# Kernel optimization log

Measured on AMD Instinct MI355X. Metric: run time of the kernel, lower is better.

## Reference

```python
import jax, jax.numpy as jnp
import numpy as np

B, N, L, H, V, LAYERS = 512, 32, 50, 256, 100000, 1


def setup_inputs() -> dict:
    key = jax.random.key(0)
    ks = jax.random.split(key, 18)
    std = 1.0 / np.sqrt(H)
    u = lambda k, shape: jax.random.uniform(k, shape, jnp.float32, -std, std)
    return {
        # forward args
        "A": jax.random.uniform(ks[0], (B, N, 2 * N), jnp.float32),
        "items": jax.random.randint(ks[1], (B, N), 0, V + 1),
        "seq_alias": jax.random.randint(ks[2], (B, L), 0, N),
        "mask": jnp.ones((B, L), jnp.int32),
        # learned parameters (uniform(-1/sqrt(H), 1/sqrt(H)) as in the module)
        "emb": u(ks[3], (V + 1, H)),
        "W_in": u(ks[4], (H, H)), "b_in": u(ks[5], (H,)),
        "W_out": u(ks[6], (H, H)), "b_out": u(ks[7], (H,)),
        "W_ih": u(ks[8], (2 * H, 3 * H)), "b_ih": u(ks[9], (3 * H,)),
        "W_hh": u(ks[10], (H, 3 * H)), "b_hh": u(ks[11], (3 * H,)),
        "fc1_w": u(ks[12], (H, H)), "fc1_b": u(ks[13], (H,)),
        "fc2_w": u(ks[14], (H, H)), "fc2_b": u(ks[15], (H,)),
        "fc3_w": u(ks[16], (H, 1)),
    }


def reference(A, items, seq_alias, mask, emb, W_in, b_in, W_out, b_out,
              W_ih, b_ih, W_hh, b_hh, fc1_w, fc1_b, fc2_w, fc2_b, fc3_w):
    # --- GGNN over dense batched adjacency A: [B, N, 2N] ---
    h = emb[items]  # [B, N, H]
    for _ in range(LAYERS):
        m_in = jnp.einsum('bij,bjh->bih', A[:, :, :N], h @ W_in + b_in)
        m_out = jnp.einsum('bij,bjh->bih', A[:, :, N:], h @ W_out + b_out)
        a = jnp.concatenate([m_in, m_out], axis=-1)  # [B, N, 2H]
        # torch.nn.GRUCell math
        gi = a @ W_ih + b_ih  # [B, N, 3H]
        gh = h @ W_hh + b_hh
        i_r, i_z, i_n = jnp.split(gi, 3, axis=-1)
        h_r, h_z, h_n = jnp.split(gh, 3, axis=-1)
        r = jax.nn.sigmoid(i_r + h_r)
        z = jax.nn.sigmoid(i_z + h_z)
        ng = jnp.tanh(i_n + r * h_n)
        h = ng + z * (h - ng)
    # --- per-sample gather of session sequences (vectorized embed_seq) ---
    h_seqs = jnp.take_along_axis(h, seq_alias[:, :, None], axis=1)  # [B, L, H]
    tail = mask.sum(axis=1) - 1  # index of last valid position
    h_tail = jnp.take_along_axis(h_seqs, tail[:, None, None], axis=1)[:, 0]  # [B, H]
    # --- attention pooling ---
    q1 = (h_tail @ fc1_w + fc1_b)[:, None, :]  # [B, 1, H]
    q2 = h_seqs @ fc2_w + fc2_b                # [B, L, H]
    alpha = jax.nn.sigmoid(q1 + q2) @ fc3_w    # [B, L, 1]
    seq_emb = jnp.sum(alpha * h_seqs * mask[:, :, None].astype(h.dtype), axis=1)  # [B, H]
    # --- score against all items (excluding padding row 0) ---
    return seq_emb @ emb[1:].T  # [B, V]
```

## Files before the change

### kernel.cpp

```cpp
#include <hip/hip_runtime.h>
#include <cmath>

#define HH 256
#define NB 32
#define LSEQ 50
#define BB 512
#define VOC 100000
#define VPAD 100032

typedef __attribute__((ext_vector_type(8))) short short8;
typedef __attribute__((ext_vector_type(4))) float f32x4;

static __device__ __forceinline__ unsigned short f2bf(float x) {
  unsigned u = __builtin_bit_cast(unsigned, x);
  u = (u + 0x7fff + ((u >> 16) & 1)) >> 16;
  return (unsigned short)u;
}
static __device__ __forceinline__ float bf2f(unsigned short h) {
  unsigned u = ((unsigned)h) << 16;
  return __builtin_bit_cast(float, u);
}
static __device__ __forceinline__ uint2 pack_hi4(float4 x, uint2& pl) {
  const unsigned short h0 = f2bf(x.x), h1 = f2bf(x.y), h2 = f2bf(x.z), h3 = f2bf(x.w);
  const unsigned short l0 = f2bf(x.x - bf2f(h0)), l1 = f2bf(x.y - bf2f(h1));
  const unsigned short l2 = f2bf(x.z - bf2f(h2)), l3 = f2bf(x.w - bf2f(h3));
  uint2 ph;
  ph.x = (unsigned)h0 | ((unsigned)h1 << 16);
  ph.y = (unsigned)h2 | ((unsigned)h3 << 16);
  pl.x = (unsigned)l0 | ((unsigned)l1 << 16);
  pl.y = (unsigned)l2 | ((unsigned)l3 << 16);
  return ph;
}

static __device__ __forceinline__ void cp16(void* lds, const void* g) {
  __builtin_amdgcn_global_load_lds(
      (const __attribute__((address_space(1))) unsigned int*)g,
      (__attribute__((address_space(3))) unsigned int*)lds, 16, 0, 0);
}

__global__ void prep_weights(const float* __restrict__ W_in, const float* __restrict__ b_in,
                             const float* __restrict__ W_out, const float* __restrict__ b_out,
                             const float* __restrict__ W_hh, const float* __restrict__ b_hh,
                             const float* __restrict__ W_ih, const float* __restrict__ fc2_w,
                             unsigned short* __restrict__ Wt_all, float* __restrict__ b_all,
                             unsigned short* __restrict__ WihT, unsigned short* __restrict__ fc2T)
{
  const int bid = blockIdx.x, k = threadIdx.x;
  if (bid < 1280) {
    const float* src; const float* bsrc; int col, nc;
    if (bid < 256)      { src = W_in;  bsrc = b_in;  col = bid;       nc = 256; }
    else if (bid < 512) { src = W_out; bsrc = b_out; col = bid - 256; nc = 256; }
    else                { src = W_hh;  bsrc = b_hh;  col = bid - 512; nc = 768; }
    Wt_all[bid * 256 + k] = f2bf(src[k * nc + col]);
    if (k == 0) b_all[bid] = bsrc[col];
  } else if (bid < 2048) {
    const int n = bid - 1280;
    WihT[n * 512 + k]       = f2bf(W_ih[k * 768 + n]);
    WihT[n * 512 + k + 256] = f2bf(W_ih[(k + 256) * 768 + n]);
  } else {
    const int n = bid - 2048;
    fc2T[n * 256 + k] = f2bf(fc2_w[k * 256 + n]);
  }
}

__global__ __launch_bounds__(256) void embsplit(const float* __restrict__ emb,
                                                unsigned short* __restrict__ ehi,
                                                unsigned short* __restrict__ elo)
{
  const int idx4 = blockIdx.x * 256 + threadIdx.x;
  const int v = idx4 >> 6, c4 = idx4 & 63;
  float4 x = make_float4(0.f, 0.f, 0.f, 0.f);
  if (v < VOC) x = *(const float4*)&emb[(size_t)(v + 1) * HH + c4 * 4];
  uint2 pl;
  const uint2 ph = pack_hi4(x, pl);
  *(uint2*)&ehi[(size_t)v * HH + c4 * 4] = ph;
  *(uint2*)&elo[(size_t)v * HH + c4 * 4] = pl;
}

__global__ __launch_bounds__(256, 3) void gemm_asplit_nt(
    const unsigned short* __restrict__ Ah, const unsigned short* __restrict__ Al,
    const unsigned short* __restrict__ Bt, const float* __restrict__ bias,
    float* __restrict__ C, int N, int K, int ldc)
{
  __shared__ unsigned short sAh[4 * 128 * 8];
  __shared__ unsigned short sAl[4 * 128 * 8];
  __shared__ unsigned short sB [4 * 128 * 8];
  const int tid = threadIdx.x;
  const int n0 = blockIdx.x * 128, m0 = blockIdx.y * 128;
  const int lane = tid & 63, wave = tid >> 6;
  const int quad = lane >> 4, l16 = lane & 15;
  const int wm = (wave >> 1) * 64, wn = (wave & 1) * 64;

  f32x4 acc[4][4];
#pragma unroll
  for (int i = 0; i < 4; ++i)
#pragma unroll
    for (int j = 0; j < 4; ++j)
#pragma unroll
      for (int r = 0; r < 4; ++r) acc[i][j][r] = 0.f;

  const int c0 = tid, c1 = tid + 256;
  const int q0 = c0 >> 7, r0 = c0 & 127;
  const int q1c = c1 >> 7, r1 = c1 & 127;

  for (int k0 = 0; k0 < K; k0 += 32) {
    const size_t ga0 = (size_t)(m0 + r0) * K + k0 + q0 * 8;
    const size_t ga1 = (size_t)(m0 + r1) * K + k0 + q1c * 8;
    const size_t gb0 = (size_t)(n0 + r0) * K + k0 + q0 * 8;
    const size_t gb1 = (size_t)(n0 + r1) * K + k0 + q1c * 8;
    cp16(&sAh[c0 * 8], &Ah[ga0]);
    cp16(&sAh[c1 * 8], &Ah[ga1]);
    cp16(&sAl[c0 * 8], &Al[ga0]);
    cp16(&sAl[c1 * 8], &Al[ga1]);
    cp16(&sB [c0 * 8], &Bt[gb0]);
    cp16(&sB [c1 * 8], &Bt[gb1]);
    __syncthreads();

    short8 fah[4], fal[4];
#pragma unroll
    for (int ms = 0; ms < 4; ++ms) {
      const int row = wm + ms * 16 + l16;
      fah[ms] = *(const short8*)&sAh[(quad * 128 + row) * 8];
      fal[ms] = *(const short8*)&sAl[(quad * 128 + row) * 8];
    }
#pragma unroll
    for (int ns = 0; ns < 4; ++ns) {
      const int col = wn + ns * 16 + l16;
      const short8 fb = *(const short8*)&sB[(quad * 128 + col) * 8];
#pragma unroll
      for (int ms = 0; ms < 4; ++ms) {
        acc[ms][ns] = __builtin_amdgcn_mfma_f32_16x16x32_bf16(fah[ms], fb, acc[ms][ns], 0, 0, 0);
        acc[ms][ns] = __builtin_amdgcn_mfma_f32_16x16x32_bf16(fal[ms], fb, acc[ms][ns], 0, 0, 0);
      }
    }
    __syncthreads();
  }

#pragma unroll
  for (int ns = 0; ns < 4; ++ns) {
    const int n = n0 + wn + ns * 16 + l16;
    const float bv = bias[n];
#pragma unroll
    for (int ms = 0; ms < 4; ++ms) {
      const int mrow = m0 + wm + ms * 16 + quad * 4;
#pragma unroll
      for (int r = 0; r < 4; ++r)
        C[(size_t)(mrow + r) * ldc + n] = acc[ms][ns][r] + bv;
    }
  }
}

#define TS 64
#define KSTEP 16
#define LDPF 68
__global__ __launch_bounds__(256) void gemm_nn_bias(
    const float* __restrict__ A, const float* __restrict__ W,
    const float* __restrict__ bias, float* __restrict__ C,
    int M, int N, int K)
{
  __shared__ float As[KSTEP * LDPF];
  __shared__ float Ws[KSTEP * LDPF];
  const int tid = threadIdx.x;
  const int tx = tid & 15, ty = tid >> 4;
  const int n0 = blockIdx.x * TS, m0 = blockIdx.y * TS;
  const int lkk = tid & 15, lm = tid >> 4;
  const int ln  = tid & 63, lkr = tid >> 6;
  float acc[4][4] = {};
  for (int k0 = 0; k0 < K; k0 += KSTEP) {
#pragma unroll
    for (int r = 0; r < 4; ++r)
      As[lkk * LDPF + lm + r * 16] = A[(m0 + lm + r * 16) * K + k0 + lkk];
#pragma unroll
    for (int r = 0; r < 4; ++r)
      Ws[(lkr + r * 4) * LDPF + ln] = W[(k0 + lkr + r * 4) * N + n0 + ln];
    __syncthreads();
#pragma unroll
    for (int kk = 0; kk < KSTEP; ++kk) {
      const float4 a4 = *(const float4*)(As + kk * LDPF + ty * 4);
      const float4 w4 = *(const float4*)(Ws + kk * LDPF + tx * 4);
      const float av[4] = {a4.x, a4.y, a4.z, a4.w};
      const float wv[4] = {w4.x, w4.y, w4.z, w4.w};
#pragma unroll
      for (int i = 0; i < 4; ++i)
#pragma unroll
        for (int j = 0; j < 4; ++j)
          acc[i][j] += av[i] * wv[j];
    }
    __syncthreads();
  }
  const float4 b4 = *(const float4*)(bias + n0 + tx * 4);
  const float bv[4] = {b4.x, b4.y, b4.z, b4.w};
#pragma unroll
  for (int i = 0; i < 4; ++i) {
    float4 o;
    o.x = acc[i][0] + bv[0]; o.y = acc[i][1] + bv[1];
    o.z = acc[i][2] + bv[2]; o.w = acc[i][3] + bv[3];
    *(float4*)(C + (m0 + ty * 4 + i) * N + n0 + tx * 4) = o;
  }
}

__global__ void gather_h0(const int* __restrict__ items, const float* __restrict__ emb,
                          float* __restrict__ h0, unsigned short* __restrict__ h0h,
                          unsigned short* __restrict__ h0l, int total4)
{
  const int e = blockIdx.x * blockDim.x + threadIdx.x;
  if (e >= total4) return;
  const int row = e >> 6, c = e & 63;
  const int it = items[row];
  const float4 x = ((const float4*)emb)[it * 64 + c];
  ((float4*)h0)[e] = x;
  uint2 pl;
  const uint2 ph = pack_hi4(x, pl);
  *(uint2*)&h0h[e * 4] = ph;
  *(uint2*)&h0l[e * 4] = pl;
}

__global__ __launch_bounds__(256) void msg_kernel(
    const float* __restrict__ A, const float* __restrict__ C1,
    unsigned short* __restrict__ ach, unsigned short* __restrict__ acl)
{
  const int b = blockIdx.x;
  const int tid = threadIdx.x;
  __shared__ float Ash[NB * 64];
#pragma unroll
  for (int r = 0; r < 8; ++r)
    Ash[tid + r * 256] = A[b * (NB * 2 * NB) + tid + r * 256];
  float hi[NB], ho[NB];
#pragma unroll
  for (int j = 0; j < NB; ++j) {
    hi[j] = C1[(size_t)(b * NB + j) * 1280 + tid];
    ho[j] = C1[(size_t)(b * NB + j) * 1280 + 256 + tid];
  }
  __syncthreads();
  for (int i = 0; i < NB; ++i) {
    float si = 0.f, so = 0.f;
#pragma unroll
    for (int j = 0; j < NB; ++j) {
      si += Ash[i * 64 + j] * hi[j];
      so += Ash[i * 64 + 32 + j] * ho[j];
    }
    const int idx = (b * NB + i) * 512 + tid;
    const unsigned short sh = f2bf(si);
    ach[idx] = sh; acl[idx] = f2bf(si - bf2f(sh));
    const unsigned short oh = f2bf(so);
    ach[idx + 256] = oh; acl[idx + 256] = f2bf(so - bf2f(oh));
  }
}

__global__ void gru_kernel(const float* __restrict__ gi, const float* __restrict__ C1,
                           float* __restrict__ h, int total)
{
  const int idx = blockIdx.x * blockDim.x + threadIdx.x;
  if (idx >= total) return;
  const int row = idx >> 8, k = idx & 255;
  const float* gir = gi + (size_t)row * 768;
  const float* ghr = C1 + (size_t)row * 1280 + 512;
  const float ir = gir[k], iz = gir[k + 256], inn = gir[k + 512];
  const float hr = ghr[k], hz = ghr[k + 256], hn = ghr[k + 512];
  const float r = 1.f / (1.f + expf(-(ir + hr)));
  const float z = 1.f / (1.f + expf(-(iz + hz)));
  const float n = tanhf(inn + r * hn);
  const float h0v = h[idx];
  h[idx] = n + z * (h0v - n);
}

__global__ __launch_bounds__(256) void seq_gather2(
    const int* __restrict__ seq_alias, const int* __restrict__ mask,
    const float* __restrict__ h, float* __restrict__ h_seqs,
    unsigned short* __restrict__ hsh, unsigned short* __restrict__ hsl,
    float* __restrict__ h_tail)
{
  const int b = blockIdx.x, tid = threadIdx.x;
  __shared__ int tail_sh;
  if (tid < 64) {
    int s = (tid < LSEQ) ? mask[b * LSEQ + tid] : 0;
#pragma unroll
    for (int off = 32; off > 0; off >>= 1) s += __shfl_down(s, off, 64);
    if (tid == 0) tail_sh = s - 1;
  }
  __syncthreads();
  const int tail = tail_sh;
  const int l0 = blockIdx.y * 10;
  for (int l = l0; l < l0 + 10; ++l) {
    const int al = seq_alias[b * LSEQ + l];
    const float v = h[(size_t)(b * NB + al) * HH + tid];
    const int idx = (b * LSEQ + l) * HH + tid;
    h_seqs[idx] = v;
    const unsigned short vh = f2bf(v);
    hsh[idx] = vh; hsl[idx] = f2bf(v - bf2f(vh));
    if (l == tail) h_tail[b * HH + tid] = v;
  }
}

__global__ __launch_bounds__(256) void attn_kernel2(
    const float* __restrict__ q1, const float* __restrict__ q2,
    const float* __restrict__ fc3_w, const float* __restrict__ h_seqs,
    const int* __restrict__ mask, float* __restrict__ seq_emb)
{
  const int b = blockIdx.x;
  const int tid = threadIdx.x, wave = tid >> 6, lane = tid & 63;
  __shared__ float red[4 * HH];
  const float4 q1v = *(const float4*)&q1[b * HH + lane * 4];
  const float4 w3v = *(const float4*)&fc3_w[lane * 4];
  float4 acc = make_float4(0.f, 0.f, 0.f, 0.f);
  for (int l = wave; l < LSEQ; l += 4) {
    if (!mask[b * LSEQ + l]) continue;
    const float4 q2v = *(const float4*)&q2[(size_t)(b * LSEQ + l) * HH + lane * 4];
    float s = (1.f / (1.f + expf(-(q1v.x + q2v.x)))) * w3v.x
            + (1.f / (1.f + expf(-(q1v.y + q2v.y)))) * w3v.y
            + (1.f / (1.f + expf(-(q1v.z + q2v.z)))) * w3v.z
            + (1.f / (1.f + expf(-(q1v.w + q2v.w)))) * w3v.w;
#pragma unroll
    for (int off = 32; off > 0; off >>= 1) s += __shfl_xor(s, off, 64);
    const float4 hv = *(const float4*)&h_seqs[(size_t)(b * LSEQ + l) * HH + lane * 4];
    acc.x += s * hv.x; acc.y += s * hv.y; acc.z += s * hv.z; acc.w += s * hv.w;
  }
  *(float4*)&red[wave * HH + lane * 4] = acc;
  __syncthreads();
  const float r = red[tid] + red[HH + tid] + red[2 * HH + tid] + red[3 * HH + tid];
  seq_emb[b * HH + tid] = r;
}

__global__ void split_seq(const float* __restrict__ s, unsigned short* __restrict__ hi,
                          unsigned short* __restrict__ lo, int n)
{
  const int i = blockIdx.x * blockDim.x + threadIdx.x;
  if (i >= n) return;
  const float x = s[i];
  const unsigned short h = f2bf(x);
  hi[i] = h;
  lo[i] = f2bf(x - bf2f(h));
}

__global__ __launch_bounds__(256, 4) void scorer_presplit(
    const unsigned short* __restrict__ seq_hi,
    const unsigned short* __restrict__ seq_lo,
    const unsigned short* __restrict__ ehi,
    const unsigned short* __restrict__ elo,
    float* __restrict__ out)
{
  const int tid = threadIdx.x;
  const int m0 = blockIdx.x * 256;
  const int v0 = blockIdx.y * 64;
  const int lane = tid & 63, wave = tid >> 6;
  const int quad = lane >> 4, l16 = lane & 15;
  const int mwave = m0 + wave * 64;

  f32x4 acc[4][4];
#pragma unroll
  for (int i = 0; i < 4; ++i)
#pragma unroll
    for (int j = 0; j < 4; ++j)
#pragma unroll
      for (int r = 0; r < 4; ++r) acc[i][j][r] = 0.f;

#pragma unroll
  for (int ks = 0; ks < 8; ++ks) {
    const int kk = ks * 32 + quad * 8;
    short8 bh[4], bl[4];
#pragma unroll
    for (int vs = 0; vs < 4; ++vs) {
      const int boff = (v0 + vs * 16 + l16) * HH + kk;
      bh[vs] = *(const short8*)&ehi[boff];
      bl[vs] = *(const short8*)&elo[boff];
    }
#pragma unroll
    for (int ms = 0; ms < 4; ++ms) {
      const int aoff = (mwave + ms * 16 + l16) * HH + kk;
      const short8 ah = *(const short8*)&seq_hi[aoff];
      const short8 al = *(const short8*)&seq_lo[aoff];
#pragma unroll
      for (int vs = 0; vs < 4; ++vs) {
        acc[ms][vs] = __builtin_amdgcn_mfma_f32_16x16x32_bf16(ah, bh[vs], acc[ms][vs], 0, 0, 0);
        acc[ms][vs] = __builtin_amdgcn_mfma_f32_16x16x32_bf16(ah, bl[vs], acc[ms][vs], 0, 0, 0);
        acc[ms][vs] = __builtin_amdgcn_mfma_f32_16x16x32_bf16(al, bh[vs], acc[ms][vs], 0, 0, 0);
      }
    }
  }

#pragma unroll
  for (int ms = 0; ms < 4; ++ms) {
    const int mrow = mwave + ms * 16 + quad * 4;
#pragma unroll
    for (int vs = 0; vs < 4; ++vs) {
      const int v = v0 + vs * 16 + l16;
      if (v < VOC) {
#pragma unroll
        for (int r = 0; r < 4; ++r)
          out[(size_t)(mrow + r) * VOC + v] = acc[ms][vs][r];
      }
    }
  }
}

#define ELD2 136
__global__ __launch_bounds__(256, 3) void scorer_mfma(
    const unsigned short* __restrict__ seq_hi,
    const unsigned short* __restrict__ seq_lo,
    const float* __restrict__ emb,
    float* __restrict__ out)
{
  __shared__ unsigned short ehi[64 * ELD2];
  __shared__ unsigned short elo[64 * ELD2];
  const int tid = threadIdx.x;
  const int v0 = blockIdx.x * 64;
  const int m0 = blockIdx.y * 256;
  const int lane = tid & 63, wave = tid >> 6;
  const int quad = lane >> 4, l16 = lane & 15;
  const int mwave = m0 + wave * 64;

  f32x4 acc[4][4];
#pragma unroll
  for (int i = 0; i < 4; ++i)
#pragma unroll
    for (int j = 0; j < 4; ++j)
#pragma unroll
      for (int r = 0; r < 4; ++r) acc[i][j][r] = 0.f;

  for (int p = 0; p < 2; ++p) {
#pragma unroll
    for (int i = 0; i < 8; ++i) {
      const int idx4 = tid + i * 256;
      const int row = idx4 >> 5, c4 = idx4 & 31;
      const int v = v0 + row;
      float4 x = make_float4(0.f, 0.f, 0.f, 0.f);
      if (v < VOC) x = *(const float4*)&emb[(size_t)(v + 1) * HH + p * 128 + c4 * 4];
      uint2 pl;
      const uint2 ph = pack_hi4(x, pl);
      *(uint2*)&ehi[row * ELD2 + c4 * 4] = ph;
      *(uint2*)&elo[row * ELD2 + c4 * 4] = pl;
    }
    __syncthreads();

#pragma unroll
    for (int ks = 0; ks < 4; ++ks) {
      const int kk = ks * 32;
      short8 bh[4], bl[4];
#pragma unroll
      for (int vs = 0; vs < 4; ++vs) {
        const int off = (vs * 16 + l16) * ELD2 + kk + quad * 8;
        bh[vs] = *(const short8*)&ehi[off];
        bl[vs] = *(const short8*)&elo[off];
      }
#pragma unroll
      for (int ms = 0; ms < 4; ++ms) {
        const int m = mwave + ms * 16 + l16;
        const int aoff = m * HH + p * 128 + kk + quad * 8;
        const short8 ah = *(const short8*)&seq_hi[aoff];
        const short8 al = *(const short8*)&seq_lo[aoff];
#pragma unroll
        for (int vs = 0; vs < 4; ++vs) {
          acc[ms][vs] = __builtin_amdgcn_mfma_f32_16x16x32_bf16(ah, bh[vs], acc[ms][vs], 0, 0, 0);
          acc[ms][vs] = __builtin_amdgcn_mfma_f32_16x16x32_bf16(ah, bl[vs], acc[ms][vs], 0, 0, 0);
          acc[ms][vs] = __builtin_amdgcn_mfma_f32_16x16x32_bf16(al, bh[vs], acc[ms][vs], 0, 0, 0);
        }
      }
    }
    __syncthreads();
  }

#pragma unroll
  for (int ms = 0; ms < 4; ++ms) {
    const int mrow = mwave + ms * 16 + quad * 4;
#pragma unroll
    for (int vs = 0; vs < 4; ++vs) {
      const int v = v0 + vs * 16 + l16;
      if (v < VOC) {
#pragma unroll
        for (int r = 0; r < 4; ++r)
          out[(size_t)(mrow + r) * VOC + v] = acc[ms][vs][r];
      }
    }
  }
}

extern "C" void kernel_launch(void* const* d_in, const int* in_sizes, int n_in,
                              void* d_out, int out_size, void* d_ws, size_t ws_size,
                              hipStream_t stream)
{
  const float* A      = (const float*)d_in[0];
  const int* items    = (const int*)d_in[1];
  const int* seq_al   = (const int*)d_in[2];
  const int* mask     = (const int*)d_in[3];
  const float* emb    = (const float*)d_in[4];
  const float* W_in   = (const float*)d_in[5];
  const float* b_in   = (const float*)d_in[6];
  const float* W_out  = (const float*)d_in[7];
  const float* b_out  = (const float*)d_in[8];
  const float* W_ih   = (const float*)d_in[9];
  const float* b_ih   = (const float*)d_in[10];
  const float* W_hh   = (const float*)d_in[11];
  const float* b_hh   = (const float*)d_in[12];
  const float* fc1_w  = (const float*)d_in[13];
  const float* fc1_b  = (const float*)d_in[14];
  const float* fc2_w  = (const float*)d_in[15];
  const float* fc2_b  = (const float*)d_in[16];
  const float* fc3_w  = (const float*)d_in[17];
  float* out = (float*)d_out;

  float* ws = (float*)d_ws;
  float* h0      = ws;
  float* q1      = ws + 4194304;
  float* h_tail  = ws + 4325376;
  float* seq_emb = ws + 4456448;
  unsigned short* seq_hi = (unsigned short*)(ws + 4587520);
  unsigned short* seq_lo = (unsigned short*)(ws + 4653056);
  unsigned short* Wt_all = (unsigned short*)(ws + 4718592);
  unsigned short* WihT   = (unsigned short*)(ws + 4882432);
  unsigned short* fc2T   = (unsigned short*)(ws + 5079040);
  float* b_all   = ws + 5111808;
  unsigned short* emb_hi = (unsigned short*)(ws + 5113088);
  unsigned short* emb_lo = (unsigned short*)(ws + 5113088 + (size_t)VPAD * HH / 2);
  const bool presplit = ws_size >= ((size_t)5113088 * 4 + (size_t)VPAD * HH * 4);

  float* C1 = out;
  unsigned short* acat_h = (unsigned short*)(out + 20971520);
  unsigned short* acat_l = (unsigned short*)(out + 25165824);
  float* gi = out + 29360128;
  unsigned short* h0h = (unsigned short*)(out + 41943040);
  unsigned short* h0l = (unsigned short*)(out + 44040192);
  float* h_seqs = out;
  unsigned short* hs_h = (unsigned short*)(out + 6553600);
  unsigned short* hs_l = (unsigned short*)(out + 9830400);
  float* q2 = out + 13107200;

  const int MR = BB * NB;

  prep_weights<<<dim3(2304), dim3(256), 0, stream>>>(
      W_in, b_in, W_out, b_out, W_hh, b_hh, W_ih, fc2_w, Wt_all, b_all, WihT, fc2T);

  if (presplit)
    embsplit<<<dim3(VPAD * 64 / 256), dim3(256), 0, stream>>>(emb, emb_hi, emb_lo);

  gather_h0<<<dim3(MR * 64 / 256), dim3(256), 0, stream>>>(items, emb, h0, h0h, h0l, MR * 64);

  gemm_asplit_nt<<<dim3(1280 / 128, MR / 128), dim3(256), 0, stream>>>(
      h0h, h0l, Wt_all, b_all, C1, 1280, 256, 1280);

  msg_kernel<<<dim3(BB), dim3(256), 0, stream>>>(A, C1, acat_h, acat_l);

  gemm_asplit_nt<<<dim3(768 / 128, MR / 128), dim3(256), 0, stream>>>(
      acat_h, acat_l, WihT, b_ih, gi, 768, 512, 768);

  gru_kernel<<<dim3(MR * HH / 256), dim3(256), 0, stream>>>(gi, C1, h0, MR * HH);

  seq_gather2<<<dim3(BB, 5), dim3(256), 0, stream>>>(seq_al, mask, h0, h_seqs, hs_h, hs_l, h_tail);

  gemm_asplit_nt<<<dim3(256 / 128, (BB * LSEQ) / 128), dim3(256), 0, stream>>>(
      hs_h, hs_l, fc2T, fc2_b, q2, 256, 256, 256);

  gemm_nn_bias<<<dim3(HH / TS, BB / TS), dim3(256), 0, stream>>>(h_tail, fc1_w, fc1_b, q1, BB, HH, HH);

  attn_kernel2<<<dim3(BB), dim3(256), 0, stream>>>(q1, q2, fc3_w, h_seqs, mask, seq_emb);

  split_seq<<<dim3(BB * HH / 256), dim3(256), 0, stream>>>(seq_emb, seq_hi, seq_lo, BB * HH);

  if (presplit)
    scorer_presplit<<<dim3(2, (VOC + 63) / 64), dim3(256), 0, stream>>>(
        seq_hi, seq_lo, emb_hi, emb_lo, out);
  else
    scorer_mfma<<<dim3((VOC + 63) / 64, 2), dim3(256), 0, stream>>>(seq_hi, seq_lo, emb, out);
}
```

Baseline: 778.6 us.

## Stage pre-split embedding tiles in swizzled LDS for the scorer GEMM

The embedding split kernel now writes hi/lo bf16 halves in a tile-contiguous, XOR-swizzled layout of 64 rows per tile. The scorer copies each tile into shared memory in two K-halves with async 16-byte copies, so the second half loads while the first is being computed. B fragments then come from bank-conflict-free LDS reads instead of scattered global loads shared across all four waves. Grid order changes so adjacent blocks walk vocabulary tiles. The larger LDS footprint lowers occupancy to 2 blocks per SM.

After: 685.0 us. -12.0%, faster.

```diff
diff --git a/kernel.cpp b/kernel.cpp
--- a/kernel.cpp
+++ b/kernel.cpp
@@ -7,6 +7,7 @@
 #define BB 512
 #define VOC 100000
 #define VPAD 100032
+#define NTILE (VPAD / 64)
 
 typedef __attribute__((ext_vector_type(8))) short short8;
 typedef __attribute__((ext_vector_type(4))) float f32x4;
@@ -63,18 +64,31 @@
   }
 }
 
-__global__ __launch_bounds__(256) void embsplit(const float* __restrict__ emb,
-                                                unsigned short* __restrict__ ehi,
-                                                unsigned short* __restrict__ elo)
-{
-  const int idx4 = blockIdx.x * 256 + threadIdx.x;
-  const int v = idx4 >> 6, c4 = idx4 & 63;
-  float4 x = make_float4(0.f, 0.f, 0.f, 0.f);
-  if (v < VOC) x = *(const float4*)&emb[(size_t)(v + 1) * HH + c4 * 4];
-  uint2 pl;
-  const uint2 ph = pack_hi4(x, pl);
-  *(uint2*)&ehi[(size_t)v * HH + c4 * 4] = ph;
-  *(uint2*)&elo[(size_t)v * HH + c4 * 4] = pl;
+__global__ __launch_bounds__(256) void embsplit_t(const float* __restrict__ emb,
+                                                  unsigned short* __restrict__ ehiT,
+                                                  unsigned short* __restrict__ eloT)
+{
+  const int g = blockIdx.x * 256 + threadIdx.x;
+  const int u = g & 1023;
+  const int tp = g >> 10;
+  const int p = tp & 1, t = tp >> 1;
+  const int row = u >> 4, w = u & 15;
+  const int wp = w ^ (row & 7);
+  const int v = t * 64 + row;
+  float4 x0 = make_float4(0.f, 0.f, 0.f, 0.f), x1 = x0;
+  if (v < VOC) {
+    const float* s = &emb[(size_t)(v + 1) * HH + p * 128 + wp * 8];
+    x0 = *(const float4*)s;
+    x1 = *(const float4*)(s + 4);
+  }
+  uint2 l0, l1;
+  const uint2 h0 = pack_hi4(x0, l0);
+  const uint2 h1 = pack_hi4(x1, l1);
+  uint4 H, L;
+  H.x = h0.x; H.y = h0.y; H.z = h1.x; H.w = h1.y;
+  L.x = l0.x; L.y = l0.y; L.z = l1.x; L.w = l1.y;
+  *(uint4*)&ehiT[(size_t)g * 8] = H;
+  *(uint4*)&eloT[(size_t)g * 8] = L;
 }
 
 __global__ __launch_bounds__(256, 3) void gemm_asplit_nt(
@@ -332,16 +346,18 @@
   lo[i] = f2bf(x - bf2f(h));
 }
 
-__global__ __launch_bounds__(256, 4) void scorer_presplit(
+__global__ __launch_bounds__(256, 2) void scorer_split_lds(
     const unsigned short* __restrict__ seq_hi,
     const unsigned short* __restrict__ seq_lo,
-    const unsigned short* __restrict__ ehi,
-    const unsigned short* __restrict__ elo,
+    const unsigned short* __restrict__ ehiT,
+    const unsigned short* __restrict__ eloT,
     float* __restrict__ out)
 {
+  __shared__ unsigned short sH[2][8192];
+  __shared__ unsigned short sL[2][8192];
   const int tid = threadIdx.x;
-  const int m0 = blockIdx.x * 256;
-  const int v0 = blockIdx.y * 64;
+  const int t = blockIdx.x;
+  const int m0 = blockIdx.y * 256;
   const int lane = tid & 63, wave = tid >> 6;
   const int quad = lane >> 4, l16 = lane & 15;
   const int mwave = m0 + wave * 64;
@@ -354,30 +370,56 @@
 #pragma unroll
       for (int r = 0; r < 4; ++r) acc[i][j][r] = 0.f;
 
-#pragma unroll
-  for (int ks = 0; ks < 8; ++ks) {
-    const int kk = ks * 32 + quad * 8;
-    short8 bh[4], bl[4];
-#pragma unroll
-    for (int vs = 0; vs < 4; ++vs) {
-      const int boff = (v0 + vs * 16 + l16) * HH + kk;
-      bh[vs] = *(const short8*)&ehi[boff];
-      bl[vs] = *(const short8*)&elo[boff];
-    }
-#pragma unroll
-    for (int ms = 0; ms < 4; ++ms) {
-      const int aoff = (mwave + ms * 16 + l16) * HH + kk;
-      const short8 ah = *(const short8*)&seq_hi[aoff];
-      const short8 al = *(const short8*)&seq_lo[aoff];
-#pragma unroll
-      for (int vs = 0; vs < 4; ++vs) {
-        acc[ms][vs] = __builtin_amdgcn_mfma_f32_16x16x32_bf16(ah, bh[vs], acc[ms][vs], 0, 0, 0);
-        acc[ms][vs] = __builtin_amdgcn_mfma_f32_16x16x32_bf16(ah, bl[vs], acc[ms][vs], 0, 0, 0);
-        acc[ms][vs] = __builtin_amdgcn_mfma_f32_16x16x32_bf16(al, bh[vs], acc[ms][vs], 0, 0, 0);
-      }
-    }
-  }
-
+  const size_t tb = (size_t)t * 16384;
+
+#pragma unroll
+  for (int j = 0; j < 4; ++j) {
+    const int o = (tid + j * 256) * 8;
+    cp16(&sH[0][o], &ehiT[tb + o]);
+    cp16(&sL[0][o], &eloT[tb + o]);
+  }
+  __syncthreads();
+
+#pragma unroll
+  for (int j = 0; j < 4; ++j) {
+    const int o = (tid + j * 256) * 8;
+    cp16(&sH[1][o], &ehiT[tb + 8192 + o]);
+    cp16(&sL[1][o], &eloT[tb + 8192 + o]);
+  }
+
+#define SCORE_PHASE(D, P)                                                          \
+  {                                                                                \
+    _Pragma("unroll")                                                              \
+    for (int ks = 0; ks < 4; ++ks) {                                               \
+      const int kk = ks * 32;                                                      \
+      short8 bh[4], bl[4];                                                         \
+      _Pragma("unroll")                                                            \
+      for (int vs = 0; vs < 4; ++vs) {                                             \
+        const int row = vs * 16 + l16;                                             \
+        const int bo = (row * 256 + (kk + quad * 8) * 2) ^ ((row & 7) << 4);       \
+        bh[vs] = *(const short8*)((const char*)&sH[D][0] + bo);                    \
+        bl[vs] = *(const short8*)((const char*)&sL[D][0] + bo);                    \
+      }                                                                            \
+      _Pragma("unroll")                                                            \
+      for (int ms = 0; ms < 4; ++ms) {                                             \
+        const int aoff = (mwave + ms * 16 + l16) * HH + (P) * 128 + kk + quad * 8; \
+        const short8 ah = *(const short8*)&seq_hi[aoff];                           \
+        const short8 al = *(const short8*)&seq_lo[aoff];                           \
+        _Pragma("unroll")                                                          \
+        for (int vs = 0; vs < 4; ++vs) {                                           \
+          acc[ms][vs] = __builtin_amdgcn_mfma_f32_16x16x32_bf16(ah, bh[vs], acc[ms][vs], 0, 0, 0); \
+          acc[ms][vs] = __builtin_amdgcn_mfma_f32_16x16x32_bf16(ah, bl[vs], acc[ms][vs], 0, 0, 0); \
+          acc[ms][vs] = __builtin_amdgcn_mfma_f32_16x16x32_bf16(al, bh[vs], acc[ms][vs], 0, 0, 0); \
+        }                                                                          \
+      }                                                                            \
+    }                                                                              \
+  }
+
+  SCORE_PHASE(0, 0)
+  __syncthreads();
+  SCORE_PHASE(1, 1)
+
+  const int v0 = t * 64;
 #pragma unroll
   for (int ms = 0; ms < 4; ++ms) {
     const int mrow = mwave + ms * 16 + quad * 4;
@@ -391,6 +433,7 @@
       }
     }
   }
+#undef SCORE_PHASE
 }
 
 #define ELD2 136
@@ -489,8 +532,8 @@
   const float* b_out  = (const float*)d_in[8];
   const float* W_ih   = (const float*)d_in[9];
   const float* b_ih   = (const float*)d_in[10];
+  const float* b_hh   = (const float*)d_in[12];
   const float* W_hh   = (const float*)d_in[11];
-  const float* b_hh   = (const float*)d_in[12];
   const float* fc1_w  = (const float*)d_in[13];
   const float* fc1_b  = (const float*)d_in[14];
   const float* fc2_w  = (const float*)d_in[15];
@@ -509,8 +552,8 @@
   unsigned short* WihT   = (unsigned short*)(ws + 4882432);
   unsigned short* fc2T   = (unsigned short*)(ws + 5079040);
   float* b_all   = ws + 5111808;
-  unsigned short* emb_hi = (unsigned short*)(ws + 5113088);
-  unsigned short* emb_lo = (unsigned short*)(ws + 5113088 + (size_t)VPAD * HH / 2);
+  unsigned short* emb_hiT = (unsigned short*)(ws + 5113088);
+  unsigned short* emb_loT = (unsigned short*)(ws + 5113088 + (size_t)VPAD * HH / 2);
   const bool presplit = ws_size >= ((size_t)5113088 * 4 + (size_t)VPAD * HH * 4);
 
   float* C1 = out;
@@ -530,7 +573,7 @@
       W_in, b_in, W_out, b_out, W_hh, b_hh, W_ih, fc2_w, Wt_all, b_all, WihT, fc2T);
 
   if (presplit)
-    embsplit<<<dim3(VPAD * 64 / 256), dim3(256), 0, stream>>>(emb, emb_hi, emb_lo);
+    embsplit_t<<<dim3(NTILE * 8), dim3(256), 0, stream>>>(emb, emb_hiT, emb_loT);
 
   gather_h0<<<dim3(MR * 64 / 256), dim3(256), 0, stream>>>(items, emb, h0, h0h, h0l, MR * 64);
 
@@ -556,8 +599,8 @@
   split_seq<<<dim3(BB * HH / 256), dim3(256), 0, stream>>>(seq_emb, seq_hi, seq_lo, BB * HH);
 
   if (presplit)
-    scorer_presplit<<<dim3(2, (VOC + 63) / 64), dim3(256), 0, stream>>>(
-        seq_hi, seq_lo, emb_hi, emb_lo, out);
+    scorer_split_lds<<<dim3(NTILE, 2), dim3(256), 0, stream>>>(
+        seq_hi, seq_lo, emb_hiT, emb_loT, out);
   else
     scorer_mfma<<<dim3((VOC + 63) / 64, 2), dim3(256), 0, stream>>>(seq_hi, seq_lo, emb, out);
 }
```
